# Performance work log

Hardware: AMD Instinct MI355X
Metric: run time of the kernel (lower is better)

## Reference

```python
import jax, jax.numpy as jnp
import numpy as np

BETA = 0.95
NUM_STEPS = 32


def setup_inputs() -> dict:
    key = jax.random.key(0)
    ks = jax.random.split(key, 6)
    B, IN, D, P = 1024, 512, 256, 8
    total = D * P
    x = jax.random.normal(ks[0], (B, IN), jnp.float32)
    W_proj = jax.random.normal(ks[1], (IN, total), jnp.float32) / np.sqrt(IN)
    b_proj = jnp.zeros((total,), jnp.float32)
    # uniform threshold distribution, sorted: linspace(0.5, 2.0, P)
    thresholds = jnp.linspace(0.5, 2.0, P, dtype=jnp.float32)
    rate_W = jax.random.normal(ks[2], (P, 1), jnp.float32) / np.sqrt(P)
    rate_b = jnp.zeros((1,), jnp.float32)
    conv1_w = jax.random.normal(ks[3], (P // 2, P, 3), jnp.float32) / np.sqrt(P * 3)
    conv1_b = jnp.zeros((P // 2,), jnp.float32)
    conv2_w = jax.random.normal(ks[4], (1, P // 2, 1), jnp.float32) / np.sqrt(P // 2)
    conv2_b = jnp.zeros((1,), jnp.float32)
    fusion = jnp.array([0.6, 0.4], jnp.float32)
    return dict(x=x, W_proj=W_proj, b_proj=b_proj, thresholds=thresholds,
                rate_W=rate_W, rate_b=rate_b, conv1_w=conv1_w, conv1_b=conv1_b,
                conv2_w=conv2_w, conv2_b=conv2_b, fusion=fusion)


def _conv1d(x, w, b):
    # x: [N, C_in, T], w: [C_out, C_in, K] -> [N, C_out, T] (SAME padding)
    y = jax.lax.conv_general_dilated(x, w, window_strides=(1,), padding='SAME',
                                     dimension_numbers=('NCH', 'OIH', 'NCH'))
    return y + b[None, :, None]


def reference(x, W_proj, b_proj, thresholds, rate_W, rate_b,
              conv1_w, conv1_b, conv2_w, conv2_b, fusion):
    B = x.shape[0]
    P = thresholds.shape[0]
    D = W_proj.shape[1] // P
    # constant input current per neuron: [B, D, P]
    I = (x @ W_proj + b_proj).reshape(B, D, P)

    # LIF recurrence (snntorch Leaky, reset_mechanism='subtract'):
    #   reset = H(mem_prev - thr); mem = beta*mem_prev + I - reset*thr; spk = H(mem - thr)
    def step(mem, _):
        reset = (mem > thresholds).astype(mem.dtype)
        mem = BETA * mem + I - reset * thresholds
        spk = (mem > thresholds).astype(mem.dtype)
        return mem, spk

    mem0 = jnp.zeros((B, D, P), x.dtype)
    _, spikes = jax.lax.scan(step, mem0, None, length=NUM_STEPS)  # [T, B, D, P]

    # rate branch
    rates = spikes.mean(axis=0)                        # [B, D, P]
    rate_dec = (rates @ rate_W)[..., 0] + rate_b[0]    # [B, D]

    # temporal branch: [B*D, P, T]
    s = jnp.transpose(spikes, (1, 2, 3, 0)).reshape(B * D, P, NUM_STEPS)
    h = jax.nn.relu(_conv1d(s, conv1_w, conv1_b))
    h = _conv1d(h, conv2_w, conv2_b)                   # [B*D, 1, T]
    temp_dec = h.mean(axis=-1).reshape(B, D)

    fw = jax.nn.softmax(fusion)
    return fw[0] * rate_dec + fw[1] * temp_dec
```

## Files before the change

kernel.cpp:

```cpp
#include <hip/hip_runtime.h>


constexpr int D_DIM   = 256;
constexpr int NTOT    = 2048;
constexpr int T_STEPS = 32;

typedef _Float16 f16x8 __attribute__((ext_vector_type(8)));
typedef _Float16 half4 __attribute__((ext_vector_type(4)));
typedef float    f32x4 __attribute__((ext_vector_type(4)));
typedef ushort   ushort8 __attribute__((ext_vector_type(8)));

#define GLOBAL_AS __attribute__((address_space(1)))
#define LDS_AS    __attribute__((address_space(3)))

__device__ __forceinline__ void split_f16(float v, ushort& h, ushort& l) {
    const _Float16 hf = (_Float16)v;
    const _Float16 lf = (_Float16)((v - (float)hf) * 2048.0f);
    h = __builtin_bit_cast(ushort, hf);
    l = __builtin_bit_cast(ushort, lf);
}

__device__ __forceinline__ void conv_x_body(const float* __restrict__ x,
                                            ushort* __restrict__ Ah,
                                            ushort* __restrict__ Al,
                                            int blk, int t)
{
    const int idx = (blk * 256 + t) * 8;
    float v[8];
    *reinterpret_cast<float4*>(v)     = *reinterpret_cast<const float4*>(x + idx);
    *reinterpret_cast<float4*>(v + 4) = *reinterpret_cast<const float4*>(x + idx + 4);
    __align__(16) ushort h[8], l[8];
#pragma unroll
    for (int j = 0; j < 8; ++j) split_f16(v[j], h[j], l[j]);
    *reinterpret_cast<ushort8*>(Ah + idx) = *reinterpret_cast<const ushort8*>(h);
    *reinterpret_cast<ushort8*>(Al + idx) = *reinterpret_cast<const ushort8*>(l);
}

__device__ __forceinline__ void conv_w_body(const float* __restrict__ Wp,
                                            ushort* __restrict__ Bh,
                                            ushort* __restrict__ Bl,
                                            float (*tile)[69],
                                            int ib, int t)
{
    const int k0 = (ib >> 5) * 64;
    const int c0 = (ib & 31) * 64;
    {
        const int r = t >> 2, cq = (t & 3) * 16;
#pragma unroll
        for (int j = 0; j < 4; ++j)
            *reinterpret_cast<float4*>(&tile[r][cq + j * 4]) =
                *reinterpret_cast<const float4*>(Wp + (size_t)(k0 + r) * NTOT + c0 + cq + j * 4);
    }
    __syncthreads();
    const int rr = t >> 2, kc2 = (t & 3) * 16;
    __align__(16) ushort h[16], l[16];
#pragma unroll
    for (int j = 0; j < 16; ++j) split_f16(tile[kc2 + j][rr], h[j], l[j]);
    ushort* dh = Bh + (size_t)(c0 + rr) * 512 + k0 + kc2;
    ushort* dl = Bl + (size_t)(c0 + rr) * 512 + k0 + kc2;
    *reinterpret_cast<ushort8*>(dh)     = *reinterpret_cast<const ushort8*>(h);
    *reinterpret_cast<ushort8*>(dh + 8) = *reinterpret_cast<const ushort8*>(h + 8);
    *reinterpret_cast<ushort8*>(dl)     = *reinterpret_cast<const ushort8*>(l);
    *reinterpret_cast<ushort8*>(dl + 8) = *reinterpret_cast<const ushort8*>(l + 8);
}

__global__ __launch_bounds__(256)
void popcode_prep(const float* __restrict__ x, const float* __restrict__ Wp,
                  ushort* __restrict__ Ah, ushort* __restrict__ Al,
                  ushort* __restrict__ Bh, ushort* __restrict__ Bl)
{
    __shared__ float tile[64][69];
    const int t = threadIdx.x;
    if (blockIdx.x < 256) conv_x_body(x, Ah, Al, blockIdx.x, t);
    else                  conv_w_body(Wp, Bh, Bl, tile, blockIdx.x - 256, t);
}

__global__ __launch_bounds__(256)
void popcode_fused(const ushort* __restrict__ Ah_g, const ushort* __restrict__ Al_g,
                   const ushort* __restrict__ Bh_g, const ushort* __restrict__ Bl_g,
                   const float* __restrict__ bp, const float* __restrict__ thrs,
                   const float* __restrict__ rateW, const float* __restrict__ rateB,
                   const float* __restrict__ c1w, const float* __restrict__ c1b,
                   const float* __restrict__ c2w, const float* __restrict__ c2b,
                   const float* __restrict__ fus, float* __restrict__ out)
{
    __shared__ __align__(16) char smem[50560];
    LDS_AS char* lds0 = (LDS_AS char*)smem;

    const int tid  = threadIdx.x;
    const int w    = tid >> 6;
    const int lane = tid & 63;

    const int wg = (blockIdx.x & 7) * 64 + (blockIdx.x >> 3);
    const int b0 = (wg & 15) * 64;
    const int c0 = (wg >> 4) * 64;

    const ushort* gbase = (w == 0) ? Ah_g : (w == 1) ? Al_g : (w == 2) ? Bh_g : Bl_g;
    const int     t0    = (w < 2) ? b0 : c0;
    const int     srow  = lane & 15;
    const int     schk  = (lane >> 4) * 8;

    const int wr = (w >> 1) * 32;
    const int wc = (w & 1) * 32;
    const int lr = lane & 15;
    const int lg = lane >> 4;

    const f32x4 zero = {0.f, 0.f, 0.f, 0.f};
    f32x4 acch[2][2] = {{zero, zero}, {zero, zero}};
    f32x4 accl[2][2] = {{zero, zero}, {zero, zero}};

    auto stage = [&](int buf, int kt) {
        const int koff = kt * 32 + schk;
#pragma unroll
        for (int i = 0; i < 4; ++i) {
            const ushort* src = gbase + (size_t)(t0 + srow + 16 * i) * 512 + koff;
            const int loff = __builtin_amdgcn_readfirstlane(buf * 16384 + w * 4096 + i * 1024);
            __builtin_amdgcn_global_load_lds((const GLOBAL_AS uint*)src,
                                             (LDS_AS uint*)(lds0 + loff), 16, 0, 0);
        }
    };

    auto compute = [&](int buf) {
        const int rbase = buf * 16384 + lane * 16;
        f16x8 ah[2], al[2], bh[2], bl[2];
#pragma unroll
        for (int m = 0; m < 2; ++m) {
            const int qa = (w >> 1) * 2 + m;
            ah[m] = *reinterpret_cast<const f16x8*>(smem + rbase +        qa * 1024);
            al[m] = *reinterpret_cast<const f16x8*>(smem + rbase + 4096 + qa * 1024);
        }
#pragma unroll
        for (int n = 0; n < 2; ++n) {
            const int qb = (w & 1) * 2 + n;
            bh[n] = *reinterpret_cast<const f16x8*>(smem + rbase +  8192 + qb * 1024);
            bl[n] = *reinterpret_cast<const f16x8*>(smem + rbase + 12288 + qb * 1024);
        }
#pragma unroll
        for (int m = 0; m < 2; ++m)
#pragma unroll
            for (int n = 0; n < 2; ++n) {
                acch[m][n] = __builtin_amdgcn_mfma_f32_16x16x32_f16(ah[m], bh[n], acch[m][n], 0, 0, 0);
                accl[m][n] = __builtin_amdgcn_mfma_f32_16x16x32_f16(al[m], bh[n], accl[m][n], 0, 0, 0);
                accl[m][n] = __builtin_amdgcn_mfma_f32_16x16x32_f16(ah[m], bl[n], accl[m][n], 0, 0, 0);
            }
    };

    float* wlds  = (float*)(smem + 50176);
    half4* lut16 = (half4*)(smem + 49408);
    if (tid < 96) wlds[tid] = c1w[tid];
    stage(0, 0);
    __syncthreads();

    if (tid < 96) {
        const int k = tid >> 5;
        const int j = (tid >> 4) & 1;
        const int n = tid & 15;
        half4 hv;
#pragma unroll
        for (int c = 0; c < 4; ++c) {
            float v = (k == 1 && j == 0) ? c1b[c] : 0.f;
#pragma unroll
            for (int p = 0; p < 4; ++p)
                v = fmaf((float)((n >> p) & 1), wlds[(c * 8 + j * 4 + p) * 3 + k], v);
            hv[c] = (_Float16)v;
        }
        lut16[tid] = hv;
    }

    for (int kt = 0; kt < 16; ++kt) {
        if (kt < 15) stage((kt + 1) & 1, kt + 1);
        compute(kt & 1);
        __syncthreads();
    }

    float* it = (float*)(smem + 32768);
    const float s = 1.0f / 2048.0f;
#pragma unroll
    for (int m = 0; m < 2; ++m)
#pragma unroll
        for (int n = 0; n < 2; ++n)
#pragma unroll
            for (int v = 0; v < 4; ++v)
                it[(wr + m * 16 + lg * 4 + v) * 65 + wc + n * 16 + lr] =
                    acch[m][n][v] + accl[m][n][v] * s;
    __syncthreads();

    float thrv[8];
#pragma unroll
    for (int p = 0; p < 8; ++p) thrv[p] = thrs[p];
    float w2c[4];
#pragma unroll
    for (int c = 0; c < 4; ++c) w2c[c] = c2w[c];
    const float f0 = fus[0], f1 = fus[1];
    const float fm = fmaxf(f0, f1);
    const float e0 = __expf(f0 - fm), e1 = __expf(f1 - fm);
    const float inv = 1.f / (e0 + e1);
    const float fw0 = e0 * inv, fw1 = e1 * inv;
    const float rb_ = rateB[0];
    const float bb2 = c2b[0];

    const int row = tid >> 2;
    for (int n2 = 0; n2 < 2; ++n2) {
        const int dloc = (tid & 3) + n2 * 4;
        const int dg   = (c0 >> 3) + dloc;

        const float* ip = it + row * 65 + dloc * 8;
        float Iv[8], mem[8];
        bool  spk[8];
        {
            const float4 bv0 = *reinterpret_cast<const float4*>(bp + dg * 8);
            const float4 bv1 = *reinterpret_cast<const float4*>(bp + dg * 8 + 4);
            Iv[0] = ip[0] + bv0.x; Iv[1] = ip[1] + bv0.y;
            Iv[2] = ip[2] + bv0.z; Iv[3] = ip[3] + bv0.w;
            Iv[4] = ip[4] + bv1.x; Iv[5] = ip[5] + bv1.y;
            Iv[6] = ip[6] + bv1.z; Iv[7] = ip[7] + bv1.w;
        }
#pragma unroll
        for (int p = 0; p < 8; ++p) { mem[p] = 0.f; spk[p] = false; }

        unsigned wrd[8] = {0u, 0u, 0u, 0u, 0u, 0u, 0u, 0u};
#pragma unroll
        for (int t = 0; t < T_STEPS; ++t) {
            unsigned by = 0u;
#pragma unroll
            for (int p = 0; p < 8; ++p) {
                const float m2 = fmaf(0.95f, mem[p], Iv[p]);
                mem[p] = spk[p] ? (m2 - thrv[p]) : m2;
                spk[p] = mem[p] > thrv[p];
                by |= spk[p] ? (1u << p) : 0u;
            }
            wrd[t >> 2] |= by << (8 * (t & 3));
        }

        float rsum = 0.f;
#pragma unroll
        for (int p = 0; p < 8; ++p) {
            const unsigned m = 0x01010101u << p;
            int cnt = 0;
#pragma unroll
            for (int q = 0; q < 8; ++q) cnt += __popc(wrd[q] & m);
            rsum = fmaf((float)cnt, rateW[p], rsum);
        }

        auto getb = [&](int t) -> unsigned {
            return (wrd[t >> 2] >> (8 * (t & 3))) & 255u;
        };
        float tacc = 0.f;
        unsigned bp_ = 0u;
        unsigned bc_ = getb(0);
#pragma unroll
        for (int t = 0; t < T_STEPS; ++t) {
            const unsigned bn_ = (t < 31) ? getb(t + 1) : 0u;
            const half4 a0 = lut16[      (bp_ & 15)];
            const half4 a1 = lut16[16 + (bp_ >> 4)];
            const half4 b0 = lut16[32 + (bc_ & 15)];
            const half4 b1 = lut16[48 + (bc_ >> 4)];
            const half4 cv0 = lut16[64 + (bn_ & 15)];
            const half4 cv1 = lut16[80 + (bn_ >> 4)];
            const half4 hsum = (a0 + a1) + ((b0 + b1) + (cv0 + cv1));
            tacc = fmaf(fmaxf((float)hsum[0], 0.f), w2c[0], tacc);
            tacc = fmaf(fmaxf((float)hsum[1], 0.f), w2c[1], tacc);
            tacc = fmaf(fmaxf((float)hsum[2], 0.f), w2c[2], tacc);
            tacc = fmaf(fmaxf((float)hsum[3], 0.f), w2c[3], tacc);
            bp_ = bc_;
            bc_ = bn_;
        }

        const float rdec = rsum * (1.f / 32.f) + rb_;
        const float temp = tacc * (1.f / 32.f) + bb2;
        out[(b0 + row) * D_DIM + dg] = fw0 * rdec + fw1 * temp;
    }
}

extern "C" void kernel_launch(void* const* d_in, const int* in_sizes, int n_in,
                              void* d_out, int out_size, void* d_ws, size_t ws_size,
                              hipStream_t stream) {
    const float* x     = (const float*)d_in[0];
    const float* Wp    = (const float*)d_in[1];
    const float* bp    = (const float*)d_in[2];
    const float* thrs  = (const float*)d_in[3];
    const float* rateW = (const float*)d_in[4];
    const float* rateB = (const float*)d_in[5];
    const float* c1w   = (const float*)d_in[6];
    const float* c1b   = (const float*)d_in[7];
    const float* c2w   = (const float*)d_in[8];
    const float* c2b   = (const float*)d_in[9];
    const float* fus   = (const float*)d_in[10];
    float* out = (float*)d_out;
    float* ws  = (float*)d_ws;

    ushort* Ah = reinterpret_cast<ushort*>(ws);
    ushort* Al = Ah + 1024 * 512;
    ushort* Bh = Al + 1024 * 512;
    ushort* Bl = Bh + 2048 * 512;

    popcode_prep<<<dim3(512), dim3(256), 0, stream>>>(x, Wp, Ah, Al, Bh, Bl);
    popcode_fused<<<dim3(512), dim3(256), 0, stream>>>(
        Ah, Al, Bh, Bl, bp, thrs, rateW, rateB, c1w, c1b, c2w, c2b, fus, out);
}
```

Baseline: 113.8 us.

## Single-buffer GEMM staging to cut LDS and change staging lane layout

Replaces the double-buffered LDS staging for the fused projection GEMM with a single buffer, shrinking shared memory so more workgroups can be resident per CU. Staging lanes now map four lanes per row with contiguous 16-byte chunks, and the compute reads use row-major offsets to match. The loop now computes, synchronises, stages the next tile, and synchronises again. This gives up overlap between global loads and MFMA work and adds an extra barrier per K step.

```diff
diff --git a/kernel.cpp b/kernel.cpp
--- a/kernel.cpp
+++ b/kernel.cpp
@@ -84,7 +84,7 @@
                    const float* __restrict__ c2w, const float* __restrict__ c2b,
                    const float* __restrict__ fus, float* __restrict__ out)
 {
-    __shared__ __align__(16) char smem[50560];
+    __shared__ __align__(16) char smem[34176];
     LDS_AS char* lds0 = (LDS_AS char*)smem;
 
     const int tid  = threadIdx.x;
@@ -97,8 +97,8 @@
 
     const ushort* gbase = (w == 0) ? Ah_g : (w == 1) ? Al_g : (w == 2) ? Bh_g : Bl_g;
     const int     t0    = (w < 2) ? b0 : c0;
-    const int     srow  = lane & 15;
-    const int     schk  = (lane >> 4) * 8;
+    const int     srow  = lane >> 2;
+    const int     schk  = (lane & 3) * 8;
 
     const int wr = (w >> 1) * 32;
     const int wc = (w & 1) * 32;
@@ -109,31 +109,30 @@
     f32x4 acch[2][2] = {{zero, zero}, {zero, zero}};
     f32x4 accl[2][2] = {{zero, zero}, {zero, zero}};
 
-    auto stage = [&](int buf, int kt) {
+    auto stage = [&](int kt) {
         const int koff = kt * 32 + schk;
 #pragma unroll
         for (int i = 0; i < 4; ++i) {
             const ushort* src = gbase + (size_t)(t0 + srow + 16 * i) * 512 + koff;
-            const int loff = __builtin_amdgcn_readfirstlane(buf * 16384 + w * 4096 + i * 1024);
+            const int loff = __builtin_amdgcn_readfirstlane(w * 4096 + i * 1024);
             __builtin_amdgcn_global_load_lds((const GLOBAL_AS uint*)src,
                                              (LDS_AS uint*)(lds0 + loff), 16, 0, 0);
         }
     };
 
-    auto compute = [&](int buf) {
-        const int rbase = buf * 16384 + lane * 16;
+    auto compute = [&]() {
         f16x8 ah[2], al[2], bh[2], bl[2];
 #pragma unroll
         for (int m = 0; m < 2; ++m) {
-            const int qa = (w >> 1) * 2 + m;
-            ah[m] = *reinterpret_cast<const f16x8*>(smem + rbase +        qa * 1024);
-            al[m] = *reinterpret_cast<const f16x8*>(smem + rbase + 4096 + qa * 1024);
+            const int ro = (wr + m * 16 + lr) * 64 + lg * 16;
+            ah[m] = *reinterpret_cast<const f16x8*>(smem +        ro);
+            al[m] = *reinterpret_cast<const f16x8*>(smem + 4096 + ro);
         }
 #pragma unroll
         for (int n = 0; n < 2; ++n) {
-            const int qb = (w & 1) * 2 + n;
-            bh[n] = *reinterpret_cast<const f16x8*>(smem + rbase +  8192 + qb * 1024);
-            bl[n] = *reinterpret_cast<const f16x8*>(smem + rbase + 12288 + qb * 1024);
+            const int co = (wc + n * 16 + lr) * 64 + lg * 16;
+            bh[n] = *reinterpret_cast<const f16x8*>(smem +  8192 + co);
+            bl[n] = *reinterpret_cast<const f16x8*>(smem + 12288 + co);
         }
 #pragma unroll
         for (int m = 0; m < 2; ++m)
@@ -145,10 +144,10 @@
             }
     };
 
-    float* wlds  = (float*)(smem + 50176);
-    half4* lut16 = (half4*)(smem + 49408);
+    float* wlds  = (float*)(smem + 33792);
+    half4* lut16 = (half4*)(smem + 33024);
     if (tid < 96) wlds[tid] = c1w[tid];
-    stage(0, 0);
+    stage(0);
     __syncthreads();
 
     if (tid < 96) {
@@ -168,12 +167,15 @@
     }
 
     for (int kt = 0; kt < 16; ++kt) {
-        if (kt < 15) stage((kt + 1) & 1, kt + 1);
-        compute(kt & 1);
+        compute();
         __syncthreads();
+        if (kt < 15) {
+            stage(kt + 1);
+            __syncthreads();
+        }
     }
 
-    float* it = (float*)(smem + 32768);
+    float* it = (float*)(smem + 16384);
     const float s = 1.0f / 2048.0f;
 #pragma unroll
     for (int m = 0; m < 2; ++m)
```

Result: faster. 111.4 us (-2.2%).

## Halve GEMM tile rows to 32x64 and double workgroup count

Applied to the files above, without the earlier changes.

Shrinks each workgroup's output tile from 64x64 to 32x64 (batch rows), doubling the grid to 1024 workgroups. The staging layout, per-wave loads and MFMA assignment are reworked: A waves load only 2 row-chunks, and each wave computes a single 16-row strip with two column tiles. The LIF epilogue drops its two-iteration loop, so each thread handles one (row, d) pair. This is meant to improve occupancy and overlap on the many CUs and to shorten the serial LIF tail per thread. The cost is more total B-tile reloads and less arithmetic per staged byte.

```diff
diff --git a/kernel.cpp b/kernel.cpp
--- a/kernel.cpp
+++ b/kernel.cpp
@@ -84,69 +84,78 @@
                    const float* __restrict__ c2w, const float* __restrict__ c2b,
                    const float* __restrict__ fus, float* __restrict__ out)
 {
-    __shared__ __align__(16) char smem[50560];
+    __shared__ __align__(16) char smem[34048];
     LDS_AS char* lds0 = (LDS_AS char*)smem;
 
     const int tid  = threadIdx.x;
     const int w    = tid >> 6;
     const int lane = tid & 63;
 
-    const int wg = (blockIdx.x & 7) * 64 + (blockIdx.x >> 3);
-    const int b0 = (wg & 15) * 64;
-    const int c0 = (wg >> 4) * 64;
-
-    const ushort* gbase = (w == 0) ? Ah_g : (w == 1) ? Al_g : (w == 2) ? Bh_g : Bl_g;
-    const int     t0    = (w < 2) ? b0 : c0;
-    const int     srow  = lane & 15;
-    const int     schk  = (lane >> 4) * 8;
-
-    const int wr = (w >> 1) * 32;
+    const int wg = ((blockIdx.x & 7) << 7) | (blockIdx.x >> 3);
+    const int b0 = (wg & 31) * 32;
+    const int c0 = (wg >> 5) * 64;
+
+    const ushort* gbase = (w == 0) ? Ah_g : (w == 3) ? Al_g : (w == 1) ? Bh_g : Bl_g;
+    const bool    isA   = (w == 0) || (w == 3);
+    const int     t0    = isA ? b0 : c0;
+    const int     pbase = (w == 0) ? 0 : (w == 3) ? 2048 : (w == 1) ? 4096 : 8192;
+    const int     srow  = lane >> 2;
+    const int     schk  = (lane & 3) * 8;
+
+    const int wr = (w >> 1) * 16;
     const int wc = (w & 1) * 32;
     const int lr = lane & 15;
     const int lg = lane >> 4;
 
     const f32x4 zero = {0.f, 0.f, 0.f, 0.f};
-    f32x4 acch[2][2] = {{zero, zero}, {zero, zero}};
-    f32x4 accl[2][2] = {{zero, zero}, {zero, zero}};
+    f32x4 acch[2] = {zero, zero};
+    f32x4 accl[2] = {zero, zero};
 
     auto stage = [&](int buf, int kt) {
         const int koff = kt * 32 + schk;
-#pragma unroll
-        for (int i = 0; i < 4; ++i) {
+        const int nb   = buf * 12288 + pbase;
+#pragma unroll
+        for (int i = 0; i < 2; ++i) {
             const ushort* src = gbase + (size_t)(t0 + srow + 16 * i) * 512 + koff;
-            const int loff = __builtin_amdgcn_readfirstlane(buf * 16384 + w * 4096 + i * 1024);
+            const int loff = __builtin_amdgcn_readfirstlane(nb + i * 1024);
             __builtin_amdgcn_global_load_lds((const GLOBAL_AS uint*)src,
                                              (LDS_AS uint*)(lds0 + loff), 16, 0, 0);
         }
+        if (!isA) {
+#pragma unroll
+            for (int i = 2; i < 4; ++i) {
+                const ushort* src = gbase + (size_t)(t0 + srow + 16 * i) * 512 + koff;
+                const int loff = __builtin_amdgcn_readfirstlane(nb + i * 1024);
+                __builtin_amdgcn_global_load_lds((const GLOBAL_AS uint*)src,
+                                                 (LDS_AS uint*)(lds0 + loff), 16, 0, 0);
+            }
+        }
     };
 
     auto compute = [&](int buf) {
-        const int rbase = buf * 16384 + lane * 16;
-        f16x8 ah[2], al[2], bh[2], bl[2];
-#pragma unroll
-        for (int m = 0; m < 2; ++m) {
-            const int qa = (w >> 1) * 2 + m;
-            ah[m] = *reinterpret_cast<const f16x8*>(smem + rbase +        qa * 1024);
-            al[m] = *reinterpret_cast<const f16x8*>(smem + rbase + 4096 + qa * 1024);
+        const int nb = buf * 12288;
+        f16x8 ah, al, bh[2], bl[2];
+        {
+            const int ro = (wr + lr) * 64 + lg * 16;
+            ah = *reinterpret_cast<const f16x8*>(smem + nb +        ro);
+            al = *reinterpret_cast<const f16x8*>(smem + nb + 2048 + ro);
         }
 #pragma unroll
         for (int n = 0; n < 2; ++n) {
-            const int qb = (w & 1) * 2 + n;
-            bh[n] = *reinterpret_cast<const f16x8*>(smem + rbase +  8192 + qb * 1024);
-            bl[n] = *reinterpret_cast<const f16x8*>(smem + rbase + 12288 + qb * 1024);
-        }
-#pragma unroll
-        for (int m = 0; m < 2; ++m)
-#pragma unroll
-            for (int n = 0; n < 2; ++n) {
-                acch[m][n] = __builtin_amdgcn_mfma_f32_16x16x32_f16(ah[m], bh[n], acch[m][n], 0, 0, 0);
-                accl[m][n] = __builtin_amdgcn_mfma_f32_16x16x32_f16(al[m], bh[n], accl[m][n], 0, 0, 0);
-                accl[m][n] = __builtin_amdgcn_mfma_f32_16x16x32_f16(ah[m], bl[n], accl[m][n], 0, 0, 0);
-            }
+            const int co = (wc + n * 16 + lr) * 64 + lg * 16;
+            bh[n] = *reinterpret_cast<const f16x8*>(smem + nb + 4096 + co);
+            bl[n] = *reinterpret_cast<const f16x8*>(smem + nb + 8192 + co);
+        }
+#pragma unroll
+        for (int n = 0; n < 2; ++n) {
+            acch[n] = __builtin_amdgcn_mfma_f32_16x16x32_f16(ah, bh[n], acch[n], 0, 0, 0);
+            accl[n] = __builtin_amdgcn_mfma_f32_16x16x32_f16(al, bh[n], accl[n], 0, 0, 0);
+            accl[n] = __builtin_amdgcn_mfma_f32_16x16x32_f16(ah, bl[n], accl[n], 0, 0, 0);
+        }
     };
 
-    float* wlds  = (float*)(smem + 50176);
-    half4* lut16 = (half4*)(smem + 49408);
+    float* wlds  = (float*)(smem + 33664);
+    half4* lut16 = (half4*)(smem + 32896);
     if (tid < 96) wlds[tid] = c1w[tid];
     stage(0, 0);
     __syncthreads();
@@ -173,16 +182,14 @@
         __syncthreads();
     }
 
-    float* it = (float*)(smem + 32768);
+    float* it = (float*)(smem + 24576);
     const float s = 1.0f / 2048.0f;
 #pragma unroll
-    for (int m = 0; m < 2; ++m)
-#pragma unroll
-        for (int n = 0; n < 2; ++n)
-#pragma unroll
-            for (int v = 0; v < 4; ++v)
-                it[(wr + m * 16 + lg * 4 + v) * 65 + wc + n * 16 + lr] =
-                    acch[m][n][v] + accl[m][n][v] * s;
+    for (int n = 0; n < 2; ++n)
+#pragma unroll
+        for (int v = 0; v < 4; ++v)
+            it[(wr + lg * 4 + v) * 65 + wc + n * 16 + lr] =
+                acch[n][v] + accl[n][v] * s;
     __syncthreads();
 
     float thrv[8];
@@ -199,77 +206,75 @@
     const float rb_ = rateB[0];
     const float bb2 = c2b[0];
 
-    const int row = tid >> 2;
-    for (int n2 = 0; n2 < 2; ++n2) {
-        const int dloc = (tid & 3) + n2 * 4;
-        const int dg   = (c0 >> 3) + dloc;
-
-        const float* ip = it + row * 65 + dloc * 8;
-        float Iv[8], mem[8];
-        bool  spk[8];
-        {
-            const float4 bv0 = *reinterpret_cast<const float4*>(bp + dg * 8);
-            const float4 bv1 = *reinterpret_cast<const float4*>(bp + dg * 8 + 4);
-            Iv[0] = ip[0] + bv0.x; Iv[1] = ip[1] + bv0.y;
-            Iv[2] = ip[2] + bv0.z; Iv[3] = ip[3] + bv0.w;
-            Iv[4] = ip[4] + bv1.x; Iv[5] = ip[5] + bv1.y;
-            Iv[6] = ip[6] + bv1.z; Iv[7] = ip[7] + bv1.w;
-        }
-#pragma unroll
-        for (int p = 0; p < 8; ++p) { mem[p] = 0.f; spk[p] = false; }
-
-        unsigned wrd[8] = {0u, 0u, 0u, 0u, 0u, 0u, 0u, 0u};
-#pragma unroll
-        for (int t = 0; t < T_STEPS; ++t) {
-            unsigned by = 0u;
-#pragma unroll
-            for (int p = 0; p < 8; ++p) {
-                const float m2 = fmaf(0.95f, mem[p], Iv[p]);
-                mem[p] = spk[p] ? (m2 - thrv[p]) : m2;
-                spk[p] = mem[p] > thrv[p];
-                by |= spk[p] ? (1u << p) : 0u;
-            }
-            wrd[t >> 2] |= by << (8 * (t & 3));
-        }
-
-        float rsum = 0.f;
+    const int row  = tid >> 3;
+    const int dloc = tid & 7;
+    const int dg   = (c0 >> 3) + dloc;
+
+    const float* ip = it + row * 65 + dloc * 8;
+    float Iv[8], mem[8];
+    bool  spk[8];
+    {
+        const float4 bv0 = *reinterpret_cast<const float4*>(bp + dg * 8);
+        const float4 bv1 = *reinterpret_cast<const float4*>(bp + dg * 8 + 4);
+        Iv[0] = ip[0] + bv0.x; Iv[1] = ip[1] + bv0.y;
+        Iv[2] = ip[2] + bv0.z; Iv[3] = ip[3] + bv0.w;
+        Iv[4] = ip[4] + bv1.x; Iv[5] = ip[5] + bv1.y;
+        Iv[6] = ip[6] + bv1.z; Iv[7] = ip[7] + bv1.w;
+    }
+#pragma unroll
+    for (int p = 0; p < 8; ++p) { mem[p] = 0.f; spk[p] = false; }
+
+    unsigned wrd[8] = {0u, 0u, 0u, 0u, 0u, 0u, 0u, 0u};
+#pragma unroll
+    for (int t = 0; t < T_STEPS; ++t) {
+        unsigned by = 0u;
 #pragma unroll
         for (int p = 0; p < 8; ++p) {
-            const unsigned m = 0x01010101u << p;
-            int cnt = 0;
-#pragma unroll
-            for (int q = 0; q < 8; ++q) cnt += __popc(wrd[q] & m);
-            rsum = fmaf((float)cnt, rateW[p], rsum);
-        }
-
-        auto getb = [&](int t) -> unsigned {
-            return (wrd[t >> 2] >> (8 * (t & 3))) & 255u;
-        };
-        float tacc = 0.f;
-        unsigned bp_ = 0u;
-        unsigned bc_ = getb(0);
-#pragma unroll
-        for (int t = 0; t < T_STEPS; ++t) {
-            const unsigned bn_ = (t < 31) ? getb(t + 1) : 0u;
-            const half4 a0 = lut16[      (bp_ & 15)];
-            const half4 a1 = lut16[16 + (bp_ >> 4)];
-            const half4 b0 = lut16[32 + (bc_ & 15)];
-            const half4 b1 = lut16[48 + (bc_ >> 4)];
-            const half4 cv0 = lut16[64 + (bn_ & 15)];
-            const half4 cv1 = lut16[80 + (bn_ >> 4)];
-            const half4 hsum = (a0 + a1) + ((b0 + b1) + (cv0 + cv1));
-            tacc = fmaf(fmaxf((float)hsum[0], 0.f), w2c[0], tacc);
-            tacc = fmaf(fmaxf((float)hsum[1], 0.f), w2c[1], tacc);
-            tacc = fmaf(fmaxf((float)hsum[2], 0.f), w2c[2], tacc);
-            tacc = fmaf(fmaxf((float)hsum[3], 0.f), w2c[3], tacc);
-            bp_ = bc_;
-            bc_ = bn_;
-        }
-
-        const float rdec = rsum * (1.f / 32.f) + rb_;
-        const float temp = tacc * (1.f / 32.f) + bb2;
-        out[(b0 + row) * D_DIM + dg] = fw0 * rdec + fw1 * temp;
-    }
+            const float m2 = fmaf(0.95f, mem[p], Iv[p]);
+            mem[p] = spk[p] ? (m2 - thrv[p]) : m2;
+            spk[p] = mem[p] > thrv[p];
+            by |= spk[p] ? (1u << p) : 0u;
+        }
+        wrd[t >> 2] |= by << (8 * (t & 3));
+    }
+
+    float rsum = 0.f;
+#pragma unroll
+    for (int p = 0; p < 8; ++p) {
+        const unsigned m = 0x01010101u << p;
+        int cnt = 0;
+#pragma unroll
+        for (int q = 0; q < 8; ++q) cnt += __popc(wrd[q] & m);
+        rsum = fmaf((float)cnt, rateW[p], rsum);
+    }
+
+    auto getb = [&](int t) -> unsigned {
+        return (wrd[t >> 2] >> (8 * (t & 3))) & 255u;
+    };
+    float tacc = 0.f;
+    unsigned bp_ = 0u;
+    unsigned bc_ = getb(0);
+#pragma unroll
+    for (int t = 0; t < T_STEPS; ++t) {
+        const unsigned bn_ = (t < 31) ? getb(t + 1) : 0u;
+        const half4 a0 = lut16[      (bp_ & 15)];
+        const half4 a1 = lut16[16 + (bp_ >> 4)];
+        const half4 b0 = lut16[32 + (bc_ & 15)];
+        const half4 b1 = lut16[48 + (bc_ >> 4)];
+        const half4 cv0 = lut16[64 + (bn_ & 15)];
+        const half4 cv1 = lut16[80 + (bn_ >> 4)];
+        const half4 hsum = (a0 + a1) + ((b0 + b1) + (cv0 + cv1));
+        tacc = fmaf(fmaxf((float)hsum[0], 0.f), w2c[0], tacc);
+        tacc = fmaf(fmaxf((float)hsum[1], 0.f), w2c[1], tacc);
+        tacc = fmaf(fmaxf((float)hsum[2], 0.f), w2c[2], tacc);
+        tacc = fmaf(fmaxf((float)hsum[3], 0.f), w2c[3], tacc);
+        bp_ = bc_;
+        bc_ = bn_;
+    }
+
+    const float rdec = rsum * (1.f / 32.f) + rb_;
+    const float temp = tacc * (1.f / 32.f) + bb2;
+    out[(b0 + row) * D_DIM + dg] = fw0 * rdec + fw1 * temp;
 }
 
 extern "C" void kernel_launch(void* const* d_in, const int* in_sizes, int n_in,
@@ -295,6 +300,6 @@
     ushort* Bl = Bh + 2048 * 512;
 
     popcode_prep<<<dim3(512), dim3(256), 0, stream>>>(x, Wp, Ah, Al, Bh, Bl);
-    popcode_fused<<<dim3(512), dim3(256), 0, stream>>>(
+    popcode_fused<<<dim3(1024), dim3(256), 0, stream>>>(
         Ah, Al, Bh, Bl, bp, thrs, rateW, rateB, c1w, c1b, c2w, c2b, fus, out);
 }
```

Measured after the change: 114.6 us. Within noise of the previous version (+0.7%).
